# Optimization experiments

Measured on AMD Instinct MI355X. Metric: run time of the kernel, lower is better.

## Reference

```python
import jax, jax.numpy as jnp
import numpy as np

D, H, DH, BLK, L, R = 768, 12, 64, 64, 2, 3  # hidden, heads, head_dim, block_size, layers, random blocks


def _ln(x, g, b):
    m = x.mean(-1, keepdims=True)
    v = ((x - m) ** 2).mean(-1, keepdims=True)
    return (x - m) * jax.lax.rsqrt(v + 1e-12) * g + b


def setup_inputs() -> dict:
    key = jax.random.key(0)
    ks = iter(jax.random.split(key, 48))
    B, S = 2, 4096
    n = S // BLK
    p = lambda *s: jax.random.normal(next(ks), s, jnp.float32) * 0.02
    inp = {
        "input_ids": jax.random.randint(next(ks), (B, S), 0, D),
        "rand_blocks": jax.random.randint(next(ks), (H, n, R), 1, n - 1),
        "emb_tok": p(D, D),
        "emb_pos": p(S, D),
        "ln_emb_g": jnp.ones((D,), jnp.float32),
        "ln_emb_b": jnp.zeros((D,), jnp.float32),
        "Wq": p(L, D, D), "bq": jnp.zeros((L, D), jnp.float32),
        "Wk": p(L, D, D), "bk": jnp.zeros((L, D), jnp.float32),
        "Wv": p(L, D, D), "bv": jnp.zeros((L, D), jnp.float32),
        "Wo": p(L, D, D), "bo": jnp.zeros((L, D), jnp.float32),
        "ln1_g": jnp.ones((L, D), jnp.float32), "ln1_b": jnp.zeros((L, D), jnp.float32),
        "W1": p(L, D, 4 * D), "b1": jnp.zeros((L, 4 * D), jnp.float32),
        "W2": p(L, 4 * D, D), "b2": jnp.zeros((L, D), jnp.float32),
        "ln2_g": jnp.ones((L, D), jnp.float32), "ln2_b": jnp.zeros((L, D), jnp.float32),
        "fc_w": p(D, 1), "fc_b": jnp.zeros((1,), jnp.float32),
    }
    return inp


def reference(input_ids, rand_blocks, emb_tok, emb_pos, ln_emb_g, ln_emb_b,
              Wq, bq, Wk, bk, Wv, bv, Wo, bo, ln1_g, ln1_b,
              W1, b1, W2, b2, ln2_g, ln2_b, fc_w, fc_b):
    B, S = input_ids.shape
    n = S // BLK
    scale = 1.0 / np.sqrt(DH).astype(np.float32)
    x = emb_tok[input_ids] + emb_pos[None, :S]
    x = _ln(x, ln_emb_g, ln_emb_b)

    # block index set per query block: global first, window (i-1,i,i+1), global last, + R random
    rows = jnp.arange(n)
    win = jnp.stack([jnp.zeros_like(rows), jnp.clip(rows - 1, 0, n - 1), rows,
                     jnp.clip(rows + 1, 0, n - 1), jnp.full_like(rows, n - 1)], axis=-1)  # [n,5]
    idx = jnp.concatenate([jnp.broadcast_to(win[None], (H, n, 5)), rand_blocks], axis=-1)  # [H,n,5+R]
    h_ar = jnp.arange(H)[:, None, None]
    K = (5 + R) * BLK

    for l in range(L):
        def heads(w, b):
            return (x @ w + b).reshape(B, S, H, DH).transpose(0, 2, 1, 3)  # [B,H,S,dh]
        q, k, v = heads(Wq[l], bq[l]), heads(Wk[l], bk[l]), heads(Wv[l], bv[l])
        qb = q.reshape(B, H, n, BLK, DH)
        kb = k.reshape(B, H, n, BLK, DH)
        vb = v.reshape(B, H, n, BLK, DH)
        gk = kb[:, h_ar, idx].reshape(B, H, n, K, DH)  # gathered key blocks
        gv = vb[:, h_ar, idx].reshape(B, H, n, K, DH)
        a = jax.nn.softmax(jnp.einsum('bhnqd,bhnkd->bhnqk', qb, gk) * scale, axis=-1)
        ctx = jnp.einsum('bhnqk,bhnkd->bhnqd', a, gv)  # [B,H,n,BLK,dh]
        # first and last query blocks attend globally (full attention rows)
        for rb in (0, n - 1):
            af = jax.nn.softmax(jnp.einsum('bhqd,bhkd->bhqk', qb[:, :, rb], k) * scale, axis=-1)
            ctx = ctx.at[:, :, rb].set(jnp.einsum('bhqk,bhkd->bhqd', af, v))
        ao = ctx.reshape(B, H, S, DH).transpose(0, 2, 1, 3).reshape(B, S, D) @ Wo[l] + bo[l]
        x = _ln(x + ao, ln1_g[l], ln1_b[l])
        ff = jax.nn.gelu(x @ W1[l] + b1[l], approximate=True) @ W2[l] + b2[l]
        x = _ln(x + ff, ln2_g[l], ln2_b[l])

    pooled = x.mean(axis=1)  # mean over sequence
    return (pooled @ fc_w + fc_b).squeeze(-1)  # [B]
```

## Files before the change

### kernel.cpp

```cpp
#include <hip/hip_runtime.h>
#include <hip/hip_bf16.h>
#include <math.h>

#define D_    768
#define H_    12
#define DH_   64
#define BLK_  64
#define L_    2
#define R_    3
#define B_    2
#define S_    4096
#define NB_   64
#define M_    (B_*S_)
#define FF_   (4*D_)
#define NCH_  8
#define QK2S_ (2*D_)

#define PSTR  72
#define SOFT_SHIFT 8.0f

typedef unsigned short u16;
typedef __bf16 bf16x8 __attribute__((ext_vector_type(8)));
typedef float  f32x4  __attribute__((ext_vector_type(4)));


__device__ inline float gelu_f(float x) {
    float y = 0.7978845608f * (x + 0.044715f * x * x * x);
    float e = __expf(2.f * y);
    float th = 1.f - 2.f / (e + 1.f);
    return 0.5f * x * (1.f + th);
}

__device__ inline u16 f2bf(float f) {
    union { __hip_bfloat16 h; u16 u; } cv;
    cv.h = __float2bfloat16(f);
    return cv.u;
}

__device__ inline float block_reduce_sum(float v, float* red) {
#pragma unroll
    for (int o = 32; o > 0; o >>= 1) v += __shfl_xor(v, o, 64);
    int wv = threadIdx.x >> 6;
    if ((threadIdx.x & 63) == 0) red[wv] = v;
    __syncthreads();
    float tot = red[0] + red[1] + red[2] + red[3];
    __syncthreads();
    return tot;
}


__global__ __launch_bounds__(256) void tcast_all_kernel(
    const float* __restrict__ Wq, const float* __restrict__ Wk,
    const float* __restrict__ Wv, const float* __restrict__ Wo,
    const float* __restrict__ W1, const float* __restrict__ W2,
    u16* __restrict__ wqkvb, u16* __restrict__ wob,
    u16* __restrict__ w1b, u16* __restrict__ w2b)
{
    __shared__ float tile[32][33];
    int idx = blockIdx.x;
    const int l = idx / 6912; idx -= l * 6912;
    const float* in; u16* outp; int K, N, x, y;
    if (idx < 2304) {
        int m = idx / 576, tt = idx % 576;
        x = tt % 24; y = tt / 24; K = D_; N = D_;
        const size_t wo = (size_t)l * D_ * D_;
        if (m == 0)      { in = Wq + wo; outp = wqkvb + (size_t)l * 3 * D_ * D_; }
        else if (m == 1) { in = Wk + wo; outp = wqkvb + (size_t)l * 3 * D_ * D_ + (size_t)D_ * D_; }
        else if (m == 2) { in = Wv + wo; outp = wqkvb + (size_t)l * 3 * D_ * D_ + (size_t)2 * D_ * D_; }
        else             { in = Wo + wo; outp = wob + wo; }
    } else if (idx < 4608) {
        int tt = idx - 2304;
        x = tt % 96; y = tt / 96; K = D_; N = FF_;
        in = W1 + (size_t)l * D_ * FF_; outp = w1b + (size_t)l * FF_ * D_;
    } else {
        int tt = idx - 4608;
        x = tt % 24; y = tt / 24; K = FF_; N = D_;
        in = W2 + (size_t)l * FF_ * D_; outp = w2b + (size_t)l * D_ * FF_;
    }
    const int n0 = x * 32, k0 = y * 32;
    const int tx = threadIdx.x & 31, ty = threadIdx.x >> 5;
#pragma unroll
    for (int p = 0; p < 4; p++)
        tile[ty + p * 8][tx] = in[(size_t)(k0 + ty + p * 8) * N + n0 + tx];
    __syncthreads();
#pragma unroll
    for (int p = 0; p < 4; p++)
        outp[(size_t)(n0 + ty + p * 8) * K + k0 + tx] = f2bf(tile[tx][ty + p * 8]);
}

__global__ __launch_bounds__(256) void bias_cat_kernel(
    const float* __restrict__ bq, const float* __restrict__ bk,
    const float* __restrict__ bv, float* __restrict__ o)
{
    int i = blockIdx.x * 256 + threadIdx.x;
    int l = i / (3 * D_), c = i % (3 * D_);
    float v = (c < D_) ? bq[(size_t)l * D_ + c]
            : (c < 2 * D_) ? bk[(size_t)l * D_ + (c - D_)]
            : bv[(size_t)l * D_ + (c - 2 * D_)];
    o[i] = v;
}


__global__ __launch_bounds__(256) void embed_ln_kernel(
    const int* __restrict__ ids, const float* __restrict__ etok,
    const float* __restrict__ epos, const float* __restrict__ g,
    const float* __restrict__ bb, float* __restrict__ x, u16* __restrict__ xb)
{
    __shared__ float red[4];
    const int tok = blockIdx.x;
    const int s   = tok & (S_ - 1);
    const int id  = ids[tok];
    const int t   = threadIdx.x;
    float v[3];
    float sum = 0.f;
#pragma unroll
    for (int i = 0; i < 3; i++) {
        int d = t + i * 256;
        v[i] = etok[(size_t)id * D_ + d] + epos[(size_t)s * D_ + d];
        sum += v[i];
    }
    float mean = block_reduce_sum(sum, red) * (1.f / 768.f);
    float sq = 0.f;
#pragma unroll
    for (int i = 0; i < 3; i++) { float dd = v[i] - mean; sq += dd * dd; }
    float var = block_reduce_sum(sq, red) * (1.f / 768.f);
    float inv = rsqrtf(var + 1e-12f);
#pragma unroll
    for (int i = 0; i < 3; i++) {
        int d = t + i * 256;
        float o = (v[i] - mean) * inv * g[d] + bb[d];
        x[(size_t)tok * D_ + d] = o;
        xb[(size_t)tok * D_ + d] = f2bf(o);
    }
}


__global__ __launch_bounds__(256) void add_ln_kernel(
    float* __restrict__ x, const float* __restrict__ y,
    const float* __restrict__ g, const float* __restrict__ bb,
    u16* __restrict__ xb)
{
    __shared__ float red[4];
    const int tok = blockIdx.x;
    const int t   = threadIdx.x;
    float* xr = x + (size_t)tok * D_;
    const float* yr = y + (size_t)tok * D_;
    float v[3];
    float sum = 0.f;
#pragma unroll
    for (int i = 0; i < 3; i++) {
        int d = t + i * 256;
        v[i] = xr[d] + yr[d];
        sum += v[i];
    }
    float mean = block_reduce_sum(sum, red) * (1.f / 768.f);
    float sq = 0.f;
#pragma unroll
    for (int i = 0; i < 3; i++) { float dd = v[i] - mean; sq += dd * dd; }
    float var = block_reduce_sum(sq, red) * (1.f / 768.f);
    float inv = rsqrtf(var + 1e-12f);
#pragma unroll
    for (int i = 0; i < 3; i++) {
        int d = t + i * 256;
        float o = (v[i] - mean) * inv * g[d] + bb[d];
        xr[d] = o;
        xb[(size_t)tok * D_ + d] = f2bf(o);
    }
}


template <int ACT, int OBF, int NN, int KK>
__global__ __launch_bounds__(256) void gemm_bf16_kernel(
    const u16* __restrict__ A, const u16* __restrict__ Wt,
    const float* __restrict__ bias, void* __restrict__ Cv)
{
    __shared__ __align__(16) u16 As[4096];
    __shared__ __align__(16) u16 Bs[4096];
    const int t = threadIdx.x;
    const int row0 = blockIdx.y * 128, col0 = blockIdx.x * 128;
    const int w = t >> 6, lane = t & 63;
    const int wr = w >> 1, wc = w & 1;
    const int i16 = lane & 15, qd = lane >> 4;

    const f32x4 zero = {0.f, 0.f, 0.f, 0.f};
    f32x4 acc[4][4];
#pragma unroll
    for (int r = 0; r < 4; r++)
#pragma unroll
        for (int c = 0; c < 4; c++) acc[r][c] = zero;

    const int e0 = t, e1 = t + 256;
    const int ra0 = e0 >> 2, ca0 = e0 & 3;
    const int ra1 = e1 >> 2, ca1 = e1 & 3;
    const int lds0 = ((ra0 >> 4) * 64 + ca0 * 16 + (ra0 & 15)) * 8;
    const int lds1 = ((ra1 >> 4) * 64 + ca1 * 16 + (ra1 & 15)) * 8;

    uint4 a0, a1, b0, b1;
    a0 = *(const uint4*)(A + (size_t)(row0 + ra0) * KK + ca0 * 8);
    a1 = *(const uint4*)(A + (size_t)(row0 + ra1) * KK + ca1 * 8);
    b0 = *(const uint4*)(Wt + (size_t)(col0 + ra0) * KK + ca0 * 8);
    b1 = *(const uint4*)(Wt + (size_t)(col0 + ra1) * KK + ca1 * 8);

    for (int k0 = 0; k0 < KK; k0 += 32) {
        __syncthreads();
        *(uint4*)&As[lds0] = a0;
        *(uint4*)&As[lds1] = a1;
        *(uint4*)&Bs[lds0] = b0;
        *(uint4*)&Bs[lds1] = b1;
        __syncthreads();
        if (k0 + 32 < KK) {
            int kn = k0 + 32;
            a0 = *(const uint4*)(A + (size_t)(row0 + ra0) * KK + kn + ca0 * 8);
            a1 = *(const uint4*)(A + (size_t)(row0 + ra1) * KK + kn + ca1 * 8);
            b0 = *(const uint4*)(Wt + (size_t)(col0 + ra0) * KK + kn + ca0 * 8);
            b1 = *(const uint4*)(Wt + (size_t)(col0 + ra1) * KK + kn + ca1 * 8);
        }
        bf16x8 af[4], bfr[4];
#pragma unroll
        for (int r = 0; r < 4; r++)
            af[r] = *(const bf16x8*)&As[(((wr * 4 + r) * 4 + qd) * 16 + i16) * 8];
#pragma unroll
        for (int c = 0; c < 4; c++)
            bfr[c] = *(const bf16x8*)&Bs[(((wc * 4 + c) * 4 + qd) * 16 + i16) * 8];
#pragma unroll
        for (int r = 0; r < 4; r++)
#pragma unroll
            for (int c = 0; c < 4; c++)
                acc[r][c] = __builtin_amdgcn_mfma_f32_16x16x32_bf16(af[r], bfr[c], acc[r][c], 0, 0, 0);
    }

#pragma unroll
    for (int c = 0; c < 4; c++) {
        int colg = col0 + wc * 64 + c * 16 + i16;
        float bsv = bias[colg];
#pragma unroll
        for (int r = 0; r < 4; r++) {
            int rowb = row0 + wr * 64 + r * 16 + qd * 4;
#pragma unroll
            for (int p = 0; p < 4; p++) {
                float val = acc[r][c][p] + bsv;
                if (ACT == 1) val = gelu_f(val);
                if (OBF == 1)
                    ((u16*)Cv)[(size_t)(rowb + p) * NN + colg] = f2bf(val);
                else
                    ((float*)Cv)[(size_t)(rowb + p) * NN + colg] = val;
            }
        }
    }
}


template <int ACT, int OBF, int NN, int KK>
__global__ __launch_bounds__(256) void gemm_bf16_n64_kernel(
    const u16* __restrict__ A, const u16* __restrict__ Wt,
    const float* __restrict__ bias, void* __restrict__ Cv)
{
    __shared__ __align__(16) u16 As[4096];
    __shared__ __align__(16) u16 Bs[2048];
    const int t = threadIdx.x;
    const int row0 = blockIdx.y * 128, col0 = blockIdx.x * 64;
    const int w = t >> 6, lane = t & 63;
    const int i16 = lane & 15, qd = lane >> 4;

    const f32x4 zero = {0.f, 0.f, 0.f, 0.f};
    f32x4 acc[2][4];
#pragma unroll
    for (int r = 0; r < 2; r++)
#pragma unroll
        for (int c = 0; c < 4; c++) acc[r][c] = zero;

    const int ra0 = t >> 2, ca = t & 3;
    const int ra1 = ra0 + 64;
    const int ldsA0 = ((ra0 >> 4) * 64 + ca * 16 + (ra0 & 15)) * 8;
    const int ldsA1 = ((ra1 >> 4) * 64 + ca * 16 + (ra1 & 15)) * 8;
    const int ldsB  = ldsA0;

    uint4 a0, a1, b0;
    a0 = *(const uint4*)(A + (size_t)(row0 + ra0) * KK + ca * 8);
    a1 = *(const uint4*)(A + (size_t)(row0 + ra1) * KK + ca * 8);
    b0 = *(const uint4*)(Wt + (size_t)(col0 + ra0) * KK + ca * 8);

    for (int k0 = 0; k0 < KK; k0 += 32) {
        __syncthreads();
        *(uint4*)&As[ldsA0] = a0;
        *(uint4*)&As[ldsA1] = a1;
        *(uint4*)&Bs[ldsB]  = b0;
        __syncthreads();
        if (k0 + 32 < KK) {
            int kn = k0 + 32;
            a0 = *(const uint4*)(A + (size_t)(row0 + ra0) * KK + kn + ca * 8);
            a1 = *(const uint4*)(A + (size_t)(row0 + ra1) * KK + kn + ca * 8);
            b0 = *(const uint4*)(Wt + (size_t)(col0 + ra0) * KK + kn + ca * 8);
        }
        bf16x8 af[2], bfr[4];
#pragma unroll
        for (int r = 0; r < 2; r++)
            af[r] = *(const bf16x8*)&As[(((w * 2 + r) * 4 + qd) * 16 + i16) * 8];
#pragma unroll
        for (int c = 0; c < 4; c++)
            bfr[c] = *(const bf16x8*)&Bs[((c * 4 + qd) * 16 + i16) * 8];
#pragma unroll
        for (int r = 0; r < 2; r++)
#pragma unroll
            for (int c = 0; c < 4; c++)
                acc[r][c] = __builtin_amdgcn_mfma_f32_16x16x32_bf16(af[r], bfr[c], acc[r][c], 0, 0, 0);
    }

#pragma unroll
    for (int c = 0; c < 4; c++) {
        int colg = col0 + c * 16 + i16;
        float bsv = bias[colg];
#pragma unroll
        for (int r = 0; r < 2; r++) {
            int rowb = row0 + w * 32 + r * 16 + qd * 4;
#pragma unroll
            for (int p = 0; p < 4; p++) {
                float val = acc[r][c][p] + bsv;
                if (ACT == 1) val = gelu_f(val);
                if (OBF == 1)
                    ((u16*)Cv)[(size_t)(rowb + p) * NN + colg] = f2bf(val);
                else
                    ((float*)Cv)[(size_t)(rowb + p) * NN + colg] = val;
            }
        }
    }
}


__global__ __launch_bounds__(256) void gemm_qkv_kernel(
    const u16* __restrict__ A, const u16* __restrict__ Wt,
    const float* __restrict__ bias, u16* __restrict__ qk, u16* __restrict__ vtg)
{
    __shared__ __align__(16) u16 As[4096];
    __shared__ __align__(16) u16 Bs[4096];
    const int t = threadIdx.x;
    const int row0 = blockIdx.y * 128, col0 = blockIdx.x * 128;
    const int w = t >> 6, lane = t & 63;
    const int wr = w >> 1, wc = w & 1;
    const int i16 = lane & 15, qd = lane >> 4;

    const f32x4 zero = {0.f, 0.f, 0.f, 0.f};
    f32x4 acc[4][4];
#pragma unroll
    for (int r = 0; r < 4; r++)
#pragma unroll
        for (int c = 0; c < 4; c++) acc[r][c] = zero;

    const int e0 = t, e1 = t + 256;
    const int ra0 = e0 >> 2, ca0 = e0 & 3;
    const int ra1 = e1 >> 2, ca1 = e1 & 3;
    const int lds0 = ((ra0 >> 4) * 64 + ca0 * 16 + (ra0 & 15)) * 8;
    const int lds1 = ((ra1 >> 4) * 64 + ca1 * 16 + (ra1 & 15)) * 8;

    uint4 a0, a1, b0, b1;
    a0 = *(const uint4*)(A + (size_t)(row0 + ra0) * D_ + ca0 * 8);
    a1 = *(const uint4*)(A + (size_t)(row0 + ra1) * D_ + ca1 * 8);
    b0 = *(const uint4*)(Wt + (size_t)(col0 + ra0) * D_ + ca0 * 8);
    b1 = *(const uint4*)(Wt + (size_t)(col0 + ra1) * D_ + ca1 * 8);

    for (int k0 = 0; k0 < D_; k0 += 32) {
        __syncthreads();
        *(uint4*)&As[lds0] = a0;
        *(uint4*)&As[lds1] = a1;
        *(uint4*)&Bs[lds0] = b0;
        *(uint4*)&Bs[lds1] = b1;
        __syncthreads();
        if (k0 + 32 < D_) {
            int kn = k0 + 32;
            a0 = *(const uint4*)(A + (size_t)(row0 + ra0) * D_ + kn + ca0 * 8);
            a1 = *(const uint4*)(A + (size_t)(row0 + ra1) * D_ + kn + ca1 * 8);
            b0 = *(const uint4*)(Wt + (size_t)(col0 + ra0) * D_ + kn + ca0 * 8);
            b1 = *(const uint4*)(Wt + (size_t)(col0 + ra1) * D_ + kn + ca1 * 8);
        }
        bf16x8 af[4], bfr[4];
#pragma unroll
        for (int r = 0; r < 4; r++)
            af[r] = *(const bf16x8*)&As[(((wr * 4 + r) * 4 + qd) * 16 + i16) * 8];
#pragma unroll
        for (int c = 0; c < 4; c++)
            bfr[c] = *(const bf16x8*)&Bs[(((wc * 4 + c) * 4 + qd) * 16 + i16) * 8];
#pragma unroll
        for (int r = 0; r < 4; r++)
#pragma unroll
            for (int c = 0; c < 4; c++)
                acc[r][c] = __builtin_amdgcn_mfma_f32_16x16x32_bf16(af[r], bfr[c], acc[r][c], 0, 0, 0);
    }

#pragma unroll
    for (int c = 0; c < 4; c++) {
        int colg = col0 + wc * 64 + c * 16 + i16;
        float bsv = bias[colg];
        if (colg < QK2S_) {
#pragma unroll
            for (int r = 0; r < 4; r++) {
                int rowb = row0 + wr * 64 + r * 16 + qd * 4;
#pragma unroll
                for (int p = 0; p < 4; p++)
                    qk[(size_t)(rowb + p) * QK2S_ + colg] = f2bf(acc[r][c][p] + bsv);
            }
        } else {
            int cv = colg - QK2S_;
            int h = cv >> 6, d = cv & 63;
#pragma unroll
            for (int r = 0; r < 4; r++) {
                int rowb = row0 + wr * 64 + r * 16 + qd * 4;
                int bb = rowb >> 12, ss = rowb & (S_ - 1);
                uint2 o;
                o.x = (unsigned)f2bf(acc[r][c][0] + bsv) | ((unsigned)f2bf(acc[r][c][1] + bsv) << 16);
                o.y = (unsigned)f2bf(acc[r][c][2] + bsv) | ((unsigned)f2bf(acc[r][c][3] + bsv) << 16);
                *(uint2*)(vtg + (((size_t)(bb * H_ + h) * DH_ + d) * S_ + ss)) = o;
            }
        }
    }
}


__device__ inline void attn_core(
    const u16* __restrict__ qtile,
    const u16* __restrict__ kbh,
    const u16* __restrict__ vth,
    const int* kbl,
    u16* Qs, u16* Ks, u16* Vs, u16* Ps,
    f32x4 (&o)[4], float (&l)[4])
{
    const int t = threadIdx.x;
    const int w = t >> 6, lane = t & 63;
    const int l15 = lane & 15, quad = lane >> 4;

    const int rsub = lane >> 3;
    const int c8w  = lane & 7;
    const int r0s  = w * 8 + rsub;
    const int r1s  = r0s + 32;
    const int soff0 = (r0s * 8 + (c8w ^ (r0s & 7))) * 8;
    const int soff1 = (r1s * 8 + (c8w ^ (r1s & 7))) * 8;

    {
        uint4 q0 = *(const uint4*)(qtile + (size_t)r0s * QK2S_ + c8w * 8);
        uint4 q1 = *(const uint4*)(qtile + (size_t)r1s * QK2S_ + c8w * 8);
        const u16* kb0 = kbh + (size_t)kbl[0] * BLK_ * QK2S_;
        const u16* vb0 = vth + kbl[0] * BLK_;
        uint4 k0 = *(const uint4*)(kb0 + (size_t)r0s * QK2S_ + c8w * 8);
        uint4 k1 = *(const uint4*)(kb0 + (size_t)r1s * QK2S_ + c8w * 8);
        uint4 v0 = *(const uint4*)(vb0 + (size_t)r0s * S_ + c8w * 8);
        uint4 v1 = *(const uint4*)(vb0 + (size_t)r1s * S_ + c8w * 8);
        *(uint4*)&Qs[soff0] = q0;  *(uint4*)&Qs[soff1] = q1;
        *(uint4*)&Ks[soff0] = k0;  *(uint4*)&Ks[soff1] = k1;
        *(uint4*)&Vs[soff0] = v0;  *(uint4*)&Vs[soff1] = v1;
    }
    __syncthreads();

    const int xq = l15 & 7;
    bf16x8 qf[2];
#pragma unroll
    for (int ki = 0; ki < 2; ki++)
        qf[ki] = *(const bf16x8*)&Qs[((w * 16 + l15) * 8 + ((ki * 4 + quad) ^ xq)) * 8];

    const f32x4 zero = {0.f, 0.f, 0.f, 0.f};
#pragma unroll
    for (int c = 0; c < 4; c++) o[c] = zero;
    float ps[4] = {0.f, 0.f, 0.f, 0.f};

    const int wxor = (quad >> 1) << 4;
    const int rxor = ((l15 >> 3) & 1) << 4;
    u16* pw = Ps + (w * 16 + quad * 4) * PSTR;
    const u16* pr = Ps + (w * 16 + l15) * PSTR;

    uint4 k0n, k1n, v0n, v1n;
#pragma unroll
    for (int kbi = 0; kbi < 8; kbi++) {
        if (kbi + 1 < 8) {
            const u16* kbn = kbh + (size_t)kbl[kbi + 1] * BLK_ * QK2S_;
            const u16* vbn = vth + kbl[kbi + 1] * BLK_;
            k0n = *(const uint4*)(kbn + (size_t)r0s * QK2S_ + c8w * 8);
            k1n = *(const uint4*)(kbn + (size_t)r1s * QK2S_ + c8w * 8);
            v0n = *(const uint4*)(vbn + (size_t)r0s * S_ + c8w * 8);
            v1n = *(const uint4*)(vbn + (size_t)r1s * S_ + c8w * 8);
        }
        const u16* Kc = Ks + (kbi & 1) * 4096;
        const u16* Vc = Vs + (kbi & 1) * 4096;
        bf16x8 kf[4][2], vf[4][2];
#pragma unroll
        for (int c = 0; c < 4; c++)
#pragma unroll
            for (int ki = 0; ki < 2; ki++) {
                const int off = ((c * 16 + l15) * 8 + ((ki * 4 + quad) ^ xq)) * 8;
                kf[c][ki] = *(const bf16x8*)&Kc[off];
                vf[c][ki] = *(const bf16x8*)&Vc[off];
            }
        f32x4 s[4];
#pragma unroll
        for (int c = 0; c < 4; c++) s[c] = zero;
#pragma unroll
        for (int ki = 0; ki < 2; ki++)
#pragma unroll
            for (int c = 0; c < 4; c++)
                s[c] = __builtin_amdgcn_mfma_f32_16x16x32_bf16(qf[ki], kf[c][ki], s[c], 0, 0, 0);
#pragma unroll
        for (int c = 0; c < 4; c++)
#pragma unroll
            for (int r = 0; r < 4; r++)
                s[c][r] = __expf(fmaf(s[c][r], 0.125f, -SOFT_SHIFT));
#pragma unroll
        for (int r = 0; r < 4; r++)
            ps[r] += (s[0][r] + s[1][r]) + (s[2][r] + s[3][r]);
#pragma unroll
        for (int c = 0; c < 4; c++) {
            const int cbase = (c * 16 + l15) ^ wxor;
#pragma unroll
            for (int r = 0; r < 4; r++)
                pw[r * PSTR + cbase] = f2bf(s[c][r]);
        }
#pragma unroll
        for (int ki = 0; ki < 2; ki++) {
            bf16x8 pf = *(const bf16x8*)(pr + ((ki * 32 + quad * 8) ^ rxor));
#pragma unroll
            for (int c = 0; c < 4; c++)
                o[c] = __builtin_amdgcn_mfma_f32_16x16x32_bf16(pf, vf[c][ki], o[c], 0, 0, 0);
        }
        if (kbi + 1 < 8) {
            u16* Kn = Ks + ((kbi + 1) & 1) * 4096;
            u16* Vn = Vs + ((kbi + 1) & 1) * 4096;
            *(uint4*)&Kn[soff0] = k0n;  *(uint4*)&Kn[soff1] = k1n;
            *(uint4*)&Vn[soff0] = v0n;  *(uint4*)&Vn[soff1] = v1n;
            __syncthreads();
        }
    }
#pragma unroll
    for (int r = 0; r < 4; r++) {
        float v = ps[r];
        v += __shfl_xor(v, 1, 16);
        v += __shfl_xor(v, 2, 16);
        v += __shfl_xor(v, 4, 16);
        v += __shfl_xor(v, 8, 16);
        l[r] = v;
    }
}


__global__ __launch_bounds__(256) void attn_kernel(
    const u16* __restrict__ qk, const u16* __restrict__ vtg,
    const int* __restrict__ rnd, u16* __restrict__ ctx,
    float* __restrict__ pctx, float* __restrict__ pl)
{
    __shared__ __align__(16) u16 Qs[4096];
    __shared__ __align__(16) u16 Ks[2 * 4096];
    __shared__ __align__(16) u16 Vs[2 * 4096];
    __shared__ __align__(16) u16 Ps[BLK_ * PSTR];

    const int hid = blockIdx.x + 78 * (blockIdx.y + H_ * blockIdx.z);
    const int lid = (hid & 7) * 234 + (hid >> 3);
    const int xk = lid % 78;
    const int yz = lid / 78;
    const int h = yz % H_;
    const int b = yz / H_;

    const int t = threadIdx.x;
    const int w = t >> 6, lane = t & 63;
    const int l15 = lane & 15, quad = lane >> 4;

    const bool sparse = (xk < 62);
    int qb, kbl[8], ci = 0;
    if (sparse) {
        qb = xk + 1;
        const int* rp = rnd + ((size_t)(h * NB_ + qb)) * R_;
        kbl[0] = 0; kbl[1] = qb - 1; kbl[2] = qb; kbl[3] = qb + 1;
        kbl[4] = NB_ - 1; kbl[5] = rp[0]; kbl[6] = rp[1]; kbl[7] = rp[2];
    } else {
        int e = xk - 62;
        int chunk = e & 7, qsel = e >> 3;
        qb = qsel ? (NB_ - 1) : 0;
#pragma unroll
        for (int i = 0; i < 8; i++) kbl[i] = chunk * 8 + i;
        ci = (((qsel * B_ + b) * H_ + h) * NCH_) + chunk;
    }

    const u16* qtile = qk + ((size_t)(b * S_ + qb * BLK_)) * QK2S_ + h * DH_;
    const u16* kbh   = qk + D_ + ((size_t)b * S_) * QK2S_ + h * DH_;
    const u16* vth   = vtg + ((size_t)(b * H_ + h) * DH_) * S_;

    f32x4 o[4]; float l[4];
    attn_core(qtile, kbh, vth, kbl, Qs, Ks, Vs, Ps, o, l);

    if (sparse) {
#pragma unroll
        for (int r = 0; r < 4; r++) {
            int row = w * 16 + quad * 4 + r;
            float inv = 1.f / l[r];
#pragma unroll
            for (int c = 0; c < 4; c++)
                ctx[((size_t)(b * S_ + qb * BLK_ + row)) * D_ + h * DH_ + c * 16 + l15] =
                    f2bf(o[c][r] * inv);
        }
    } else {
#pragma unroll
        for (int r = 0; r < 4; r++) {
            int row = w * 16 + quad * 4 + r;
#pragma unroll
            for (int c = 0; c < 4; c++)
                pctx[((size_t)ci * BLK_ + row) * DH_ + c * 16 + l15] = o[c][r];
            if (l15 == 0)
                pl[(size_t)ci * BLK_ + row] = l[r];
        }
    }
}

__global__ __launch_bounds__(256) void attn_combine_kernel(
    const float* __restrict__ pctx, const float* __restrict__ pl,
    u16* __restrict__ ctx)
{
    const int qsel = blockIdx.x, h = blockIdx.y, b = blockIdx.z;
    const int qb = qsel ? (NB_ - 1) : 0;
    const int t = threadIdx.x;
    const int row = t >> 2, q4 = t & 3;
    const int cbase = ((qsel * B_ + b) * H_ + h) * NCH_;

    float L = 0.f;
#pragma unroll
    for (int c = 0; c < NCH_; c++) L += pl[(size_t)(cbase + c) * BLK_ + row];

    float acc[16];
#pragma unroll
    for (int j = 0; j < 16; j++) acc[j] = 0.f;
#pragma unroll
    for (int c = 0; c < NCH_; c++) {
        const float* src = pctx + ((size_t)(cbase + c) * BLK_ + row) * DH_ + q4 * 16;
#pragma unroll
        for (int jj = 0; jj < 4; jj++) {
            float4 f = *(const float4*)(src + jj * 4);
            acc[jj * 4 + 0] += f.x;
            acc[jj * 4 + 1] += f.y;
            acc[jj * 4 + 2] += f.z;
            acc[jj * 4 + 3] += f.w;
        }
    }
    float invL = 1.f / L;
    u16* dst = ctx + ((size_t)(b * S_ + qb * BLK_ + row)) * D_ + h * DH_ + q4 * 16;
    uint4 o0, o1;
#pragma unroll
    for (int g = 0; g < 8; g++) {
        unsigned lo = (unsigned)f2bf(acc[g * 2 + 0] * invL);
        unsigned hi = (unsigned)f2bf(acc[g * 2 + 1] * invL);
        unsigned pk = lo | (hi << 16);
        if (g < 4) (&o0.x)[g] = pk; else (&o1.x)[g - 4] = pk;
    }
    *(uint4*)dst = o0;
    *(uint4*)(dst + 8) = o1;
}


__global__ __launch_bounds__(256) void pool_kernel(
    const float* __restrict__ x, const float* __restrict__ fcw,
    float* __restrict__ acc)
{
    __shared__ float red[4];
    const int chunk = blockIdx.x, b = blockIdx.y;
    const int t = threadIdx.x;
    float s = 0.f;
    for (int sr = 0; sr < 128; sr++) {
        const float* xr = x + ((size_t)(b * S_ + chunk * 128 + sr)) * D_;
#pragma unroll
        for (int i = 0; i < 3; i++) {
            int d = t + i * 256;
            s += xr[d] * fcw[d];
        }
    }
    float tot = block_reduce_sum(s, red);
    if (t == 0) atomicAdd(&acc[b], tot);
}

__global__ void final_kernel(const float* __restrict__ acc,
                             const float* __restrict__ fcb,
                             float* __restrict__ out)
{
    if (threadIdx.x < B_) out[threadIdx.x] = acc[threadIdx.x] * (1.f / S_) + fcb[0];
}


extern "C" void kernel_launch(void* const* d_in, const int* in_sizes, int n_in,
                              void* d_out, int out_size, void* d_ws, size_t ws_size,
                              hipStream_t stream)
{
    (void)in_sizes; (void)n_in; (void)out_size; (void)ws_size;
    const int*   ids  = (const int*)d_in[0];
    const int*   rnd  = (const int*)d_in[1];
    const float* etok = (const float*)d_in[2];
    const float* epos = (const float*)d_in[3];
    const float* lng  = (const float*)d_in[4];
    const float* lnb  = (const float*)d_in[5];
    const float* Wq   = (const float*)d_in[6];
    const float* bq   = (const float*)d_in[7];
    const float* Wk   = (const float*)d_in[8];
    const float* bk   = (const float*)d_in[9];
    const float* Wv   = (const float*)d_in[10];
    const float* bv   = (const float*)d_in[11];
    const float* Wo   = (const float*)d_in[12];
    const float* bo   = (const float*)d_in[13];
    const float* ln1g = (const float*)d_in[14];
    const float* ln1b = (const float*)d_in[15];
    const float* W1   = (const float*)d_in[16];
    const float* b1   = (const float*)d_in[17];
    const float* W2   = (const float*)d_in[18];
    const float* b2   = (const float*)d_in[19];
    const float* ln2g = (const float*)d_in[20];
    const float* ln2b = (const float*)d_in[21];
    const float* fcw  = (const float*)d_in[22];
    const float* fcb  = (const float*)d_in[23];
    float* out = (float*)d_out;

    const size_t MD = (size_t)M_ * D_;
    const size_t PCTX = (size_t)2 * B_ * H_ * NCH_ * BLK_ * DH_;
    const size_t PML  = (size_t)2 * B_ * H_ * NCH_ * BLK_;

    float* x     = (float*)d_ws;
    float* regB  = x + MD;
    float* pctx  = regB + MD;
    float* pl    = pctx + PCTX;
    u16*   qkb   = (u16*)(pl + PML);
    u16*   vtg   = qkb + 2 * MD;
    u16*   ctxb  = vtg + MD;
    u16*   ffhb  = qkb;
    u16*   xb    = ctxb + MD;
    u16*   wqkvb = xb + MD;
    u16*   wob   = wqkvb + (size_t)L_ * 3 * D_ * D_;
    u16*   w1b   = wob + (size_t)L_ * D_ * D_;
    u16*   w2b   = w1b + (size_t)L_ * FF_ * D_;
    float* bqkv  = (float*)(w2b + (size_t)L_ * D_ * FF_);
    float* acc   = bqkv + (size_t)L_ * 3 * D_;

    hipMemsetAsync(acc, 0, 2 * sizeof(float), stream);

    tcast_all_kernel<<<L_ * 6912, 256, 0, stream>>>(
        Wq, Wk, Wv, Wo, W1, W2, wqkvb, wob, w1b, w2b);
    bias_cat_kernel<<<(L_ * 3 * D_) / 256, 256, 0, stream>>>(bq, bk, bv, bqkv);
    embed_ln_kernel<<<M_, 256, 0, stream>>>(ids, etok, epos, lng, lnb, x, xb);

    dim3 gQKV(3 * D_ / 128, M_ / 128);
    dim3 gN64(D_ / 64, M_ / 128);
    dim3 gF(FF_ / 128, M_ / 128);
    for (int l = 0; l < L_; l++) {
        const size_t wo = (size_t)l * D_ * D_;
        const size_t vo = (size_t)l * D_;
        gemm_qkv_kernel<<<gQKV, 256, 0, stream>>>(
            xb, wqkvb + (size_t)l * 3 * D_ * D_, bqkv + (size_t)l * 3 * D_, qkb, vtg);
        attn_kernel<<<dim3(78, H_, B_), 256, 0, stream>>>(qkb, vtg, rnd, ctxb, pctx, pl);
        attn_combine_kernel<<<dim3(2, H_, B_), 256, 0, stream>>>(pctx, pl, ctxb);
        gemm_bf16_n64_kernel<0, 0, D_, D_><<<gN64, 256, 0, stream>>>(ctxb, wob + wo, bo + vo, regB);
        add_ln_kernel<<<M_, 256, 0, stream>>>(x, regB, ln1g + vo, ln1b + vo, xb);
        gemm_bf16_kernel<1, 1, FF_, D_><<<gF, 256, 0, stream>>>(
            xb, w1b + (size_t)l * FF_ * D_, b1 + (size_t)l * FF_, ffhb);
        gemm_bf16_n64_kernel<0, 0, D_, FF_><<<gN64, 256, 0, stream>>>(
            ffhb, w2b + (size_t)l * D_ * FF_, b2 + vo, regB);
        add_ln_kernel<<<M_, 256, 0, stream>>>(x, regB, ln2g + vo, ln2b + vo, xb);
    }
    pool_kernel<<<dim3(S_ / 128, B_), 256, 0, stream>>>(x, fcw, acc);
    final_kernel<<<1, 64, 0, stream>>>(acc, fcb, out);
}
```

Measured before the change: 818.9 us.

## Double-buffer LDS tiles in GEMMs and remap blocks across XCDs

The three bf16 GEMM kernels now keep two shared-memory tile buffers, so the next K-slice is written to the spare buffer after the MFMAs. This leaves one barrier per iteration instead of two. Block indices are also remapped so that consecutive logical tiles land on the same XCD, to improve L2 reuse of A/B panels. This doubles LDS use per block, which may lower occupancy. The remap assumes the grid size is divisible by 8.

```diff
diff --git a/kernel.cpp b/kernel.cpp
--- a/kernel.cpp
+++ b/kernel.cpp
@@ -46,6 +46,12 @@
     float tot = red[0] + red[1] + red[2] + red[3];
     __syncthreads();
     return tot;
+}
+
+__device__ inline int xcd_lid() {
+    const int hid = blockIdx.y * gridDim.x + blockIdx.x;
+    const int chunk = (gridDim.x * gridDim.y) >> 3;
+    return (hid & 7) * chunk + (hid >> 3);
 }
 
 
@@ -174,10 +180,12 @@
     const u16* __restrict__ A, const u16* __restrict__ Wt,
     const float* __restrict__ bias, void* __restrict__ Cv)
 {
-    __shared__ __align__(16) u16 As[4096];
-    __shared__ __align__(16) u16 Bs[4096];
+    __shared__ __align__(16) u16 As[2][4096];
+    __shared__ __align__(16) u16 Bs[2][4096];
     const int t = threadIdx.x;
-    const int row0 = blockIdx.y * 128, col0 = blockIdx.x * 128;
+    const int gx = gridDim.x;
+    const int lid = xcd_lid();
+    const int row0 = (lid / gx) * 128, col0 = (lid % gx) * 128;
     const int w = t >> 6, lane = t & 63;
     const int wr = w >> 1, wc = w & 1;
     const int i16 = lane & 15, qd = lane >> 4;
@@ -200,15 +208,17 @@
     a1 = *(const uint4*)(A + (size_t)(row0 + ra1) * KK + ca1 * 8);
     b0 = *(const uint4*)(Wt + (size_t)(col0 + ra0) * KK + ca0 * 8);
     b1 = *(const uint4*)(Wt + (size_t)(col0 + ra1) * KK + ca1 * 8);
-
+    *(uint4*)&As[0][lds0] = a0;
+    *(uint4*)&As[0][lds1] = a1;
+    *(uint4*)&Bs[0][lds0] = b0;
+    *(uint4*)&Bs[0][lds1] = b1;
+    __syncthreads();
+
+#pragma unroll 2
     for (int k0 = 0; k0 < KK; k0 += 32) {
-        __syncthreads();
-        *(uint4*)&As[lds0] = a0;
-        *(uint4*)&As[lds1] = a1;
-        *(uint4*)&Bs[lds0] = b0;
-        *(uint4*)&Bs[lds1] = b1;
-        __syncthreads();
-        if (k0 + 32 < KK) {
+        const int buf = (k0 >> 5) & 1;
+        const bool more = (k0 + 32 < KK);
+        if (more) {
             int kn = k0 + 32;
             a0 = *(const uint4*)(A + (size_t)(row0 + ra0) * KK + kn + ca0 * 8);
             a1 = *(const uint4*)(A + (size_t)(row0 + ra1) * KK + kn + ca1 * 8);
@@ -218,15 +228,22 @@
         bf16x8 af[4], bfr[4];
 #pragma unroll
         for (int r = 0; r < 4; r++)
-            af[r] = *(const bf16x8*)&As[(((wr * 4 + r) * 4 + qd) * 16 + i16) * 8];
+            af[r] = *(const bf16x8*)&As[buf][(((wr * 4 + r) * 4 + qd) * 16 + i16) * 8];
 #pragma unroll
         for (int c = 0; c < 4; c++)
-            bfr[c] = *(const bf16x8*)&Bs[(((wc * 4 + c) * 4 + qd) * 16 + i16) * 8];
+            bfr[c] = *(const bf16x8*)&Bs[buf][(((wc * 4 + c) * 4 + qd) * 16 + i16) * 8];
 #pragma unroll
         for (int r = 0; r < 4; r++)
 #pragma unroll
             for (int c = 0; c < 4; c++)
                 acc[r][c] = __builtin_amdgcn_mfma_f32_16x16x32_bf16(af[r], bfr[c], acc[r][c], 0, 0, 0);
+        if (more) {
+            *(uint4*)&As[buf ^ 1][lds0] = a0;
+            *(uint4*)&As[buf ^ 1][lds1] = a1;
+            *(uint4*)&Bs[buf ^ 1][lds0] = b0;
+            *(uint4*)&Bs[buf ^ 1][lds1] = b1;
+            __syncthreads();
+        }
     }
 
 #pragma unroll
@@ -255,10 +272,12 @@
     const u16* __restrict__ A, const u16* __restrict__ Wt,
     const float* __restrict__ bias, void* __restrict__ Cv)
 {
-    __shared__ __align__(16) u16 As[4096];
-    __shared__ __align__(16) u16 Bs[2048];
+    __shared__ __align__(16) u16 As[2][4096];
+    __shared__ __align__(16) u16 Bs[2][2048];
     const int t = threadIdx.x;
-    const int row0 = blockIdx.y * 128, col0 = blockIdx.x * 64;
+    const int gx = gridDim.x;
+    const int lid = xcd_lid();
+    const int row0 = (lid / gx) * 128, col0 = (lid % gx) * 64;
     const int w = t >> 6, lane = t & 63;
     const int i16 = lane & 15, qd = lane >> 4;
 
@@ -279,14 +298,16 @@
     a0 = *(const uint4*)(A + (size_t)(row0 + ra0) * KK + ca * 8);
     a1 = *(const uint4*)(A + (size_t)(row0 + ra1) * KK + ca * 8);
     b0 = *(const uint4*)(Wt + (size_t)(col0 + ra0) * KK + ca * 8);
-
+    *(uint4*)&As[0][ldsA0] = a0;
+    *(uint4*)&As[0][ldsA1] = a1;
+    *(uint4*)&Bs[0][ldsB]  = b0;
+    __syncthreads();
+
+#pragma unroll 2
     for (int k0 = 0; k0 < KK; k0 += 32) {
-        __syncthreads();
-        *(uint4*)&As[ldsA0] = a0;
-        *(uint4*)&As[ldsA1] = a1;
-        *(uint4*)&Bs[ldsB]  = b0;
-        __syncthreads();
-        if (k0 + 32 < KK) {
+        const int buf = (k0 >> 5) & 1;
+        const bool more = (k0 + 32 < KK);
+        if (more) {
             int kn = k0 + 32;
             a0 = *(const uint4*)(A + (size_t)(row0 + ra0) * KK + kn + ca * 8);
             a1 = *(const uint4*)(A + (size_t)(row0 + ra1) * KK + kn + ca * 8);
@@ -295,15 +316,21 @@
         bf16x8 af[2], bfr[4];
 #pragma unroll
         for (int r = 0; r < 2; r++)
-            af[r] = *(const bf16x8*)&As[(((w * 2 + r) * 4 + qd) * 16 + i16) * 8];
+            af[r] = *(const bf16x8*)&As[buf][(((w * 2 + r) * 4 + qd) * 16 + i16) * 8];
 #pragma unroll
         for (int c = 0; c < 4; c++)
-            bfr[c] = *(const bf16x8*)&Bs[((c * 4 + qd) * 16 + i16) * 8];
+            bfr[c] = *(const bf16x8*)&Bs[buf][((c * 4 + qd) * 16 + i16) * 8];
 #pragma unroll
         for (int r = 0; r < 2; r++)
 #pragma unroll
             for (int c = 0; c < 4; c++)
                 acc[r][c] = __builtin_amdgcn_mfma_f32_16x16x32_bf16(af[r], bfr[c], acc[r][c], 0, 0, 0);
+        if (more) {
+            *(uint4*)&As[buf ^ 1][ldsA0] = a0;
+            *(uint4*)&As[buf ^ 1][ldsA1] = a1;
+            *(uint4*)&Bs[buf ^ 1][ldsB]  = b0;
+            __syncthreads();
+        }
     }
 
 #pragma unroll
@@ -331,10 +358,12 @@
     const u16* __restrict__ A, const u16* __restrict__ Wt,
     const float* __restrict__ bias, u16* __restrict__ qk, u16* __restrict__ vtg)
 {
-    __shared__ __align__(16) u16 As[4096];
-    __shared__ __align__(16) u16 Bs[4096];
+    __shared__ __align__(16) u16 As[2][4096];
+    __shared__ __align__(16) u16 Bs[2][4096];
     const int t = threadIdx.x;
-    const int row0 = blockIdx.y * 128, col0 = blockIdx.x * 128;
+    const int gx = gridDim.x;
+    const int lid = xcd_lid();
+    const int row0 = (lid / gx) * 128, col0 = (lid % gx) * 128;
     const int w = t >> 6, lane = t & 63;
     const int wr = w >> 1, wc = w & 1;
     const int i16 = lane & 15, qd = lane >> 4;
@@ -357,15 +386,17 @@
     a1 = *(const uint4*)(A + (size_t)(row0 + ra1) * D_ + ca1 * 8);
     b0 = *(const uint4*)(Wt + (size_t)(col0 + ra0) * D_ + ca0 * 8);
     b1 = *(const uint4*)(Wt + (size_t)(col0 + ra1) * D_ + ca1 * 8);
-
+    *(uint4*)&As[0][lds0] = a0;
+    *(uint4*)&As[0][lds1] = a1;
+    *(uint4*)&Bs[0][lds0] = b0;
+    *(uint4*)&Bs[0][lds1] = b1;
+    __syncthreads();
+
+#pragma unroll 2
     for (int k0 = 0; k0 < D_; k0 += 32) {
-        __syncthreads();
-        *(uint4*)&As[lds0] = a0;
-        *(uint4*)&As[lds1] = a1;
-        *(uint4*)&Bs[lds0] = b0;
-        *(uint4*)&Bs[lds1] = b1;
-        __syncthreads();
-        if (k0 + 32 < D_) {
+        const int buf = (k0 >> 5) & 1;
+        const bool more = (k0 + 32 < D_);
+        if (more) {
             int kn = k0 + 32;
             a0 = *(const uint4*)(A + (size_t)(row0 + ra0) * D_ + kn + ca0 * 8);
             a1 = *(const uint4*)(A + (size_t)(row0 + ra1) * D_ + kn + ca1 * 8);
@@ -375,15 +406,22 @@
         bf16x8 af[4], bfr[4];
 #pragma unroll
         for (int r = 0; r < 4; r++)
-            af[r] = *(const bf16x8*)&As[(((wr * 4 + r) * 4 + qd) * 16 + i16) * 8];
+            af[r] = *(const bf16x8*)&As[buf][(((wr * 4 + r) * 4 + qd) * 16 + i16) * 8];
 #pragma unroll
         for (int c = 0; c < 4; c++)
-            bfr[c] = *(const bf16x8*)&Bs[(((wc * 4 + c) * 4 + qd) * 16 + i16) * 8];
+            bfr[c] = *(const bf16x8*)&Bs[buf][(((wc * 4 + c) * 4 + qd) * 16 + i16) * 8];
 #pragma unroll
         for (int r = 0; r < 4; r++)
 #pragma unroll
             for (int c = 0; c < 4; c++)
                 acc[r][c] = __builtin_amdgcn_mfma_f32_16x16x32_bf16(af[r], bfr[c], acc[r][c], 0, 0, 0);
+        if (more) {
+            *(uint4*)&As[buf ^ 1][lds0] = a0;
+            *(uint4*)&As[buf ^ 1][lds1] = a1;
+            *(uint4*)&Bs[buf ^ 1][lds0] = b0;
+            *(uint4*)&Bs[buf ^ 1][lds1] = b1;
+            __syncthreads();
+        }
     }
 
 #pragma unroll
```

Measured after the change: 745.0 us. 9.0% less time.
